# Kernel tuning notes

Hardware: AMD Instinct MI355X
Metric: run time of the kernel (lower is better)

Reference implementation:

```python
import jax, jax.numpy as jnp
import numpy as np


def rotary_pos_emb(x):
    # x: [b, h, l, k]; interleaved rotary embedding (pairs are (0,1),(2,3),...)
    dim = x.shape[-1]
    seq = x.shape[-2]
    ts = jnp.arange(0, dim, 2, dtype=jnp.float32)
    inv_freqs = 10000.0 ** (-ts / dim)                      # [dim/2]
    grid = jnp.arange(seq, dtype=jnp.float32)[:, None] * inv_freqs[None, :]  # [l, dim/2]
    sin_embs = jnp.repeat(jnp.sin(grid), 2, axis=-1)[None]  # [1, l, dim] (interleaved repeat)
    cos_embs = jnp.repeat(jnp.cos(grid), 2, axis=-1)[None]
    x1, x2 = x[..., ::2], x[..., 1::2]
    xs = jnp.stack([-x2, x1], axis=-1).reshape(x.shape)     # interleave (-x2, x1)
    return x * cos_embs + xs * sin_embs


def setup_inputs() -> dict:
    key = jax.random.key(0)
    ks = jax.random.split(key, 5)
    b, l, d = 2, 2048, 1024
    scale = 1.0 / np.sqrt(d)
    return {
        "x": jax.random.normal(ks[0], (b, l, d), dtype=jnp.float32),
        "Wq": jax.random.normal(ks[1], (d, d), dtype=jnp.float32) * scale,
        "Wk": jax.random.normal(ks[2], (d, d), dtype=jnp.float32) * scale,
        "Wv": jax.random.normal(ks[3], (d, d), dtype=jnp.float32) * scale,
        "Wo": jax.random.normal(ks[4], (d, d), dtype=jnp.float32) * scale,
        "is_training": 0,
    }


def reference(x, Wq, Wk, Wv, Wo, is_training):
    n_heads = 16
    b, l, d = x.shape
    k_size = d // n_heads
    # NOTE: module scales q by 1/sqrt(model_size), not 1/sqrt(key_size)
    q = (x @ Wq) / jnp.sqrt(jnp.float32(d))
    q = q.reshape(b, l, n_heads, k_size).transpose(0, 2, 1, 3)  # b h l k
    k = (x @ Wk).reshape(b, l, n_heads, k_size).transpose(0, 2, 1, 3)
    v = (x @ Wv).reshape(b, l, n_heads, k_size).transpose(0, 2, 1, 3)
    q = rotary_pos_emb(q)
    k = rotary_pos_emb(k)
    logits = jnp.einsum('bhik,bhjk->bhij', q, k)  # no mask, no dropout (eval)
    a = jax.nn.softmax(logits, axis=-1)
    y = jnp.einsum('bhij,bhjv->bhiv', a, v)
    y = y.transpose(0, 2, 1, 3).reshape(b, l, d)  # b l (h v)
    return y @ Wo
```

## Files before the change

kernel.cpp:

```cpp
#include <hip/hip_runtime.h>
#include <stdint.h>

typedef unsigned short u16;
typedef unsigned int u32;
using short8 = __attribute__((ext_vector_type(8))) short;
using f32x4  = __attribute__((ext_vector_type(4))) float;
using f32x16 = __attribute__((ext_vector_type(16))) float;

typedef __attribute__((address_space(1))) unsigned int gu32;
typedef __attribute__((address_space(3))) unsigned int lu32;

__device__ __forceinline__ void gl2lds16(const u16* g, u16* lds_wave_base) {
    __builtin_amdgcn_global_load_lds(
        (gu32*)(uintptr_t)(const void*)g,
        (lu32*)(uint32_t)(uintptr_t)(void*)lds_wave_base,
        16, 0, 0);
}

__device__ inline float bf2f(u16 u) {
    union { unsigned int i; float f; } v;
    v.i = ((unsigned int)u) << 16;
    return v.f;
}
__device__ inline u16 f2bf(float f) {
    union { float f; unsigned int i; } v;
    v.f = f;
    unsigned int x = v.i;
    return (u16)((x + 0x7fffu + ((x >> 16) & 1u)) >> 16);
}
__device__ inline u32 f2bf_trunc_u32(float f) {
    union { float f; unsigned int i; } v;
    v.f = f;
    return v.i >> 16;
}

__global__ __launch_bounds__(256) void prep(
    const float* __restrict__ x, u16* __restrict__ xb,
    const float* __restrict__ w0, const float* __restrict__ w1,
    const float* __restrict__ w2, const float* __restrict__ w3,
    u16* __restrict__ t0, u16* __restrict__ t1,
    u16* __restrict__ t2, u16* __restrict__ t3,
    float2* __restrict__ tab)
{
    int tx = threadIdx.x, ty = threadIdx.y;
    int tid = ty * 32 + tx;
    int z = blockIdx.z;
    if (z == 4) {
        int bidx = blockIdx.y * 32 + blockIdx.x;
        if (bidx < 256) {
            int idx = bidx * 256 + tid;
            int pos = idx >> 5, pi = idx & 31;
            const float l2_10000_over_32 = 0.41524101186f;
            float ang = (float)pos *
                __builtin_amdgcn_exp2f(-(float)pi * l2_10000_over_32);
            float sn, cs;
            __sincosf(ang, &sn, &cs);
            tab[idx] = make_float2(cs, sn);
        }
        return;
    }
    if (z >= 5) {
        int i = (((z - 5) * 1024 + blockIdx.y * 32 + blockIdx.x) * 256 + tid) * 4;
        float4 v = *(const float4*)(x + i);
        ushort4 o;
        o.x = f2bf(v.x); o.y = f2bf(v.y); o.z = f2bf(v.z); o.w = f2bf(v.w);
        *(ushort4*)(xb + i) = o;
        return;
    }
    __shared__ u16 tile[32][33];
    const float* src; u16* dst;
    switch (z) {
        case 0:  src = w0; dst = t0; break;
        case 1:  src = w1; dst = t1; break;
        case 2:  src = w2; dst = t2; break;
        default: src = w3; dst = t3; break;
    }
    int c0 = blockIdx.x * 32, r0 = blockIdx.y * 32;
    #pragma unroll
    for (int i = 0; i < 4; i++)
        tile[ty + i * 8][tx] = f2bf(src[(size_t)(r0 + ty + i * 8) * 1024 + c0 + tx]);
    __syncthreads();
    #pragma unroll
    for (int i = 0; i < 4; i++)
        dst[(size_t)(c0 + ty + i * 8) * 1024 + r0 + tx] = tile[tx][ty + i * 8];
}

__global__ __launch_bounds__(256) void gemm_qkv(
    const u16* __restrict__ A, const u16* __restrict__ Bt,
    const float2* __restrict__ ropetab,
    u16* __restrict__ Qb, u16* __restrict__ Kb, u16* __restrict__ VT)
{
    __shared__ __align__(16) char smem[24576];
    u16* As = (u16*)smem;
    u16* Bs = (u16*)(smem + 16384);

    const int tid  = threadIdx.x;
    const int lane = tid & 63;
    const int wid  = tid >> 6;
    const int quad = lane >> 4;
    const int l15  = lane & 15;
    const int wm   = wid >> 1, wn = wid & 1;

    const int m0 = blockIdx.y * 128;
    const int n0 = blockIdx.x * 64;
    const int mat = n0 >> 10;
    const int ln0 = n0 & 1023;

    f32x4 acc[4][2] = {};

    for (int k0 = 0; k0 < 1024; k0 += 64) {
        #pragma unroll
        for (int it = 0; it < 4; it++) {
            int c   = it * 256 + tid;
            int row = c >> 3;
            int col = ((c & 7) ^ (row & 7)) * 8;
            gl2lds16(&A[(size_t)(m0 + row) * 1024 + k0 + col],
                     &As[(size_t)(it * 256 + wid * 64) * 8]);
        }
        #pragma unroll
        for (int it = 0; it < 2; it++) {
            int c   = it * 256 + tid;
            int row = c >> 3;
            int col = ((c & 7) ^ (row & 7)) * 8;
            gl2lds16(&Bt[(size_t)(n0 + row) * 1024 + k0 + col],
                     &Bs[(size_t)(it * 256 + wid * 64) * 8]);
        }
        __syncthreads();

        #pragma unroll
        for (int s = 0; s < 2; s++) {
            short8 a[4], b[2];
            #pragma unroll
            for (int i = 0; i < 4; i++) {
                int ra = wm * 64 + i * 16 + l15;
                a[i] = *(const short8*)(&As[ra * 64 + (((s * 4 + quad) ^ (ra & 7)) * 8)]);
            }
            #pragma unroll
            for (int j = 0; j < 2; j++) {
                int rb = wn * 32 + j * 16 + l15;
                b[j] = *(const short8*)(&Bs[rb * 64 + (((s * 4 + quad) ^ (rb & 7)) * 8)]);
            }
            #pragma unroll
            for (int i = 0; i < 4; i++)
                #pragma unroll
                for (int j = 0; j < 2; j++)
                    acc[i][j] = __builtin_amdgcn_mfma_f32_16x16x32_bf16(a[i], b[j], acc[i][j], 0, 0, 0);
        }
        __syncthreads();
    }

    if (mat < 2) {
        u16* C = (mat == 0) ? Qb : Kb;
        const float scale = (mat == 0) ? (0.03125f * 1.44269504f) : 1.0f;
        const int odd = l15 & 1;
        #pragma unroll
        for (int i = 0; i < 4; i++)
            #pragma unroll
            for (int j = 0; j < 2; j++)
                #pragma unroll
                for (int r = 0; r < 4; r++) {
                    int lrow = wm * 64 + i * 16 + quad * 4 + r;
                    int col  = ln0 + wn * 32 + j * 16 + l15;
                    int pos  = (m0 + lrow) & 2047;
                    float v  = acc[i][j][r] * scale;
                    float vp = __shfl_xor(v, 1);
                    float2 sc = ropetab[pos * 32 + ((col & 63) >> 1)];
                    float outv = odd ? (v * sc.x + vp * sc.y)
                                     : (v * sc.x - vp * sc.y);
                    C[(size_t)(m0 + lrow) * 1024 + col] = f2bf(outv);
                }
    } else {
        u16* T = (u16*)smem;
        __syncthreads();
        const int qp = ((quad & 1) << 1) | (quad >> 1);
        #pragma unroll
        for (int i = 0; i < 4; i++)
            #pragma unroll
            for (int j = 0; j < 2; j++)
                #pragma unroll
                for (int r = 0; r < 4; r++) {
                    int prow = wm * 64 + i * 16 + qp * 4 + r;
                    int lcol = wn * 32 + j * 16 + l15;
                    T[lcol * 136 + prow] = f2bf(acc[i][j][r]);
                }
        __syncthreads();
        int bb2 = m0 >> 11, pos0 = m0 & 2047, h2 = ln0 >> 6;
        #pragma unroll
        for (int itc = 0; itc < 4; itc++) {
            int c  = itc * 256 + tid;
            int ch = c >> 4;
            int px = (c & 15) * 8;
            size_t dst = ((size_t)(bb2 * 16 + h2) * 64 + ch) * 2048
                         + pos0 + px;
            *(uint4*)(&VT[dst]) = *(const uint4*)(&T[ch * 136 + px]);
        }
    }
}

__global__ __launch_bounds__(256) void gemm_out(
    const u16* __restrict__ A, const u16* __restrict__ Bt, float* __restrict__ C)
{
    __shared__ __align__(16) u16 As[64 * 64];
    __shared__ __align__(16) u16 Bs[64 * 64];

    const int tid  = threadIdx.x;
    const int lane = tid & 63;
    const int wid  = tid >> 6;
    const int quad = lane >> 4;
    const int l15  = lane & 15;
    const int wm   = wid >> 1, wn = wid & 1;

    const int m0 = blockIdx.y * 64;
    const int n0 = blockIdx.x * 64;

    f32x4 acc[2][2] = {};

    for (int k0 = 0; k0 < 1024; k0 += 64) {
        #pragma unroll
        for (int it = 0; it < 2; it++) {
            int c   = it * 256 + tid;
            int row = c >> 3;
            int col = ((c & 7) ^ (row & 7)) * 8;
            gl2lds16(&A[(size_t)(m0 + row) * 1024 + k0 + col],
                     &As[(size_t)(it * 256 + wid * 64) * 8]);
        }
        #pragma unroll
        for (int it = 0; it < 2; it++) {
            int c   = it * 256 + tid;
            int row = c >> 3;
            int col = ((c & 7) ^ (row & 7)) * 8;
            gl2lds16(&Bt[(size_t)(n0 + row) * 1024 + k0 + col],
                     &Bs[(size_t)(it * 256 + wid * 64) * 8]);
        }
        __syncthreads();

        #pragma unroll
        for (int s = 0; s < 2; s++) {
            short8 a[2], b[2];
            #pragma unroll
            for (int i = 0; i < 2; i++) {
                int ra = wm * 32 + i * 16 + l15;
                a[i] = *(const short8*)(&As[ra * 64 + (((s * 4 + quad) ^ (ra & 7)) * 8)]);
            }
            #pragma unroll
            for (int j = 0; j < 2; j++) {
                int rb = wn * 32 + j * 16 + l15;
                b[j] = *(const short8*)(&Bs[rb * 64 + (((s * 4 + quad) ^ (rb & 7)) * 8)]);
            }
            #pragma unroll
            for (int i = 0; i < 2; i++)
                #pragma unroll
                for (int j = 0; j < 2; j++)
                    acc[i][j] = __builtin_amdgcn_mfma_f32_16x16x32_bf16(a[i], b[j], acc[i][j], 0, 0, 0);
        }
        __syncthreads();
    }

    #pragma unroll
    for (int i = 0; i < 2; i++)
        #pragma unroll
        for (int j = 0; j < 2; j++)
            #pragma unroll
            for (int r = 0; r < 4; r++) {
                int row = m0 + wm * 32 + i * 16 + quad * 4 + r;
                int col = n0 + wn * 32 + j * 16 + l15;
                C[(size_t)row * 1024 + col] = acc[i][j][r];
            }
}

__global__ __launch_bounds__(256, 2) void attn(
    const u16* __restrict__ Q, const u16* __restrict__ Kb,
    const u16* __restrict__ VT, u16* __restrict__ Y)
{
    __shared__ __align__(16) u16 Ks [128 * 68];
    __shared__ __align__(16) u16 VTs[64 * 128];

    const int tid  = threadIdx.x;
    const int lane = tid & 63, wid = tid >> 6;
    const int l31  = lane & 31, hi = lane >> 5;

    const int bh = blockIdx.x;
    const int qt = blockIdx.y;
    const int bb = bh >> 4, h = bh & 15;

    const size_t base = ((size_t)bb * 2048) * 1024 + (size_t)h * 64;

    short8 qf[4];
    {
        const u16* qp = Q + base
                      + ((size_t)qt * 128 + wid * 32 + l31) * 1024 + hi * 8;
        #pragma unroll
        for (int s = 0; s < 4; s++)
            qf[s] = *(const short8*)(qp + s * 16);
    }

    const int c0 = tid,        c1 = 256 + tid,
              c2 = 512 + tid,  c3 = 768 + tid;
    const int rk0 = c0 >> 3, ck0 = ((c0 & 7) ^ (rk0 & 7)) * 8;
    const int rk1 = c1 >> 3, ck1 = ((c1 & 7) ^ (rk1 & 7)) * 8;
    const int rk2 = c2 >> 3, ck2 = ((c2 & 7) ^ (rk2 & 7)) * 8;
    const int rk3 = c3 >> 3, ck3 = ((c3 & 7) ^ (rk3 & 7)) * 8;
    const int rv0 = c0 >> 4, cv0 = ((c0 & 15) ^ (rv0 & 15)) * 8;
    const int rv1 = c1 >> 4, cv1 = ((c1 & 15) ^ (rv1 & 15)) * 8;
    const int rv2 = c2 >> 4, cv2 = ((c2 & 15) ^ (rv2 & 15)) * 8;
    const int rv3 = c3 >> 4, cv3 = ((c3 & 15) ^ (rv3 & 15)) * 8;
    const int dK0 = rk0 * 68 + (c0 & 7) * 8, dK1 = rk1 * 68 + (c1 & 7) * 8;
    const int dK2 = rk2 * 68 + (c2 & 7) * 8, dK3 = rk3 * 68 + (c3 & 7) * 8;
    const u16* pK = Kb + base;
    const u16* pV = VT + ((size_t)bh * 64) * 2048;
    const size_t oK0 = (size_t)rk0 * 1024 + ck0, oK1 = (size_t)rk1 * 1024 + ck1;
    const size_t oK2 = (size_t)rk2 * 1024 + ck2, oK3 = (size_t)rk3 * 1024 + ck3;
    const size_t oV0 = (size_t)rv0 * 2048 + cv0, oV1 = (size_t)rv1 * 2048 + cv1;
    const size_t oV2 = (size_t)rv2 * 2048 + cv2, oV3 = (size_t)rv3 * 2048 + cv3;

    uint4 k0r, k1r, k2r, k3r, v0r, v1r, v2r, v3r;
#define LOADREGS(J0)                                                        \
    do {                                                                    \
        const size_t jk = (size_t)(J0) * 1024;                              \
        k0r = *(const uint4*)(pK + jk + oK0);                               \
        k1r = *(const uint4*)(pK + jk + oK1);                               \
        k2r = *(const uint4*)(pK + jk + oK2);                               \
        k3r = *(const uint4*)(pK + jk + oK3);                               \
        v0r = *(const uint4*)(pV + (J0) + oV0);                             \
        v1r = *(const uint4*)(pV + (J0) + oV1);                             \
        v2r = *(const uint4*)(pV + (J0) + oV2);                             \
        v3r = *(const uint4*)(pV + (J0) + oV3);                             \
    } while (0)

    f32x16 o0 = {}, o1 = {};
    float lsum = 0.0f;

    LOADREGS(0);

    for (int j0 = 0; j0 < 2048; j0 += 128) {
        __syncthreads();
        *(uint4*)(&Ks [dK0]) = k0r;
        *(uint4*)(&Ks [dK1]) = k1r;
        *(uint4*)(&Ks [dK2]) = k2r;
        *(uint4*)(&Ks [dK3]) = k3r;
        *(uint4*)(&VTs[(0 * 256 + tid) * 8]) = v0r;
        *(uint4*)(&VTs[(1 * 256 + tid) * 8]) = v1r;
        *(uint4*)(&VTs[(2 * 256 + tid) * 8]) = v2r;
        *(uint4*)(&VTs[(3 * 256 + tid) * 8]) = v3r;
        if (j0 + 128 < 2048)
            LOADREGS(j0 + 128);
        __syncthreads();

        f32x16 st[4];
        #pragma unroll
        for (int t = 0; t < 4; t++) {
            int key = t * 32 + l31;
            f32x16 z = {};
            __builtin_amdgcn_s_setprio(1);
            #pragma unroll
            for (int s = 0; s < 4; s++) {
                int chunk = ((2 * s + hi) ^ (key & 7)) * 8;
                short8 kf = *(const short8*)(&Ks[key * 68 + chunk]);
                z = __builtin_amdgcn_mfma_f32_32x32x16_bf16(kf, qf[s], z, 0, 0, 0);
            }
            __builtin_amdgcn_s_setprio(0);
            st[t] = z;
        }

        u32 X[4][4], Y[4][4];
        #pragma unroll
        for (int t = 0; t < 4; t++)
            #pragma unroll
            for (int g = 0; g < 4; g++) {
                float p0 = __builtin_amdgcn_exp2f(st[t][4 * g + 0]);
                float p1 = __builtin_amdgcn_exp2f(st[t][4 * g + 1]);
                float p2 = __builtin_amdgcn_exp2f(st[t][4 * g + 2]);
                float p3 = __builtin_amdgcn_exp2f(st[t][4 * g + 3]);
                lsum += (p0 + p1) + (p2 + p3);
                X[t][g] = f2bf_trunc_u32(p0) | (f2bf_trunc_u32(p1) << 16);
                Y[t][g] = f2bf_trunc_u32(p2) | (f2bf_trunc_u32(p3) << 16);
            }

        #pragma unroll
        for (int c16 = 0; c16 < 8; ++c16) {
            const int t = c16 >> 1, u = c16 & 1;
            union { u32 u4[4]; short8 s8; } pk;
            pk.u4[0] = X[t][2 * u];
            pk.u4[1] = Y[t][2 * u];
            pk.u4[2] = X[t][2 * u + 1];
            pk.u4[3] = Y[t][2 * u + 1];
            const int kch = 2 * c16 + hi;
            short8 v0 = *(const short8*)(&VTs[l31 * 128 + ((kch ^ (l31 & 15)) * 8)]);
            short8 v1 = *(const short8*)(&VTs[(32 + l31) * 128 + ((kch ^ ((32 + l31) & 15)) * 8)]);
            __builtin_amdgcn_s_setprio(1);
            o0 = __builtin_amdgcn_mfma_f32_32x32x16_bf16(pk.s8, v0, o0, 0, 0, 0);
            o1 = __builtin_amdgcn_mfma_f32_32x32x16_bf16(pk.s8, v1, o1, 0, 0, 0);
            __builtin_amdgcn_s_setprio(0);
        }
    }
#undef LOADREGS

    lsum += __shfl_xor(lsum, 32);
    float linv = 1.0f / lsum;

    size_t qrow0 = (size_t)qt * 128 + wid * 32;
    #pragma unroll
    for (int half = 0; half < 2; half++) {
        f32x16 o = half ? o1 : o0;
        #pragma unroll
        for (int reg = 0; reg < 16; reg++) {
            int qrow = (reg & 3) + 8 * (reg >> 2) + 4 * hi;
            float nv = o[reg] * __shfl(linv, qrow);
            Y[base + (qrow0 + qrow) * 1024 + half * 32 + l31] = f2bf(nv);
        }
    }
}

extern "C" void kernel_launch(void* const* d_in, const int* in_sizes, int n_in,
                              void* d_out, int out_size, void* d_ws, size_t ws_size,
                              hipStream_t stream)
{
    const float* x  = (const float*)d_in[0];
    const float* Wq = (const float*)d_in[1];
    const float* Wk = (const float*)d_in[2];
    const float* Wv = (const float*)d_in[3];
    const float* Wo = (const float*)d_in[4];
    float* out = (float*)d_out;

    char* ws = (char*)d_ws;
    u16*    xb    = (u16*)   (ws + (0ull  << 20));
    u16*    WqkvT = (u16*)   (ws + (8ull  << 20));
    u16*    WoT   = (u16*)   (ws + (14ull << 20));
    u16*    Qb    = (u16*)   (ws + (16ull << 20));
    u16*    Kb    = (u16*)   (ws + (24ull << 20));
    u16*    VTb   = (u16*)   (ws + (32ull << 20));
    u16*    Yb    = (u16*)   (ws + (40ull << 20));
    float2* tab   = (float2*)(ws + (48ull << 20));

    prep<<<dim3(32, 32, 9), dim3(32, 8), 0, stream>>>(
        x, xb, Wq, Wk, Wv, Wo,
        WqkvT, WqkvT + (1024ull * 1024), WqkvT + (2048ull * 1024), WoT, tab);
    gemm_qkv<<<dim3(48, 32), 256, 0, stream>>>(xb, WqkvT, tab, Qb, Kb, VTb);
    attn<<<dim3(32, 16), 256, 0, stream>>>(Qb, Kb, VTb, Yb);
    gemm_out<<<dim3(16, 64), 256, 0, stream>>>(Yb, WoT, out);
}
```

Baseline: 181.7 us.

## Double-buffer K/V tiles in LDS to halve barriers in attention loop

```diff
diff --git a/kernel.cpp b/kernel.cpp
--- a/kernel.cpp
+++ b/kernel.cpp
@@ -272,8 +272,10 @@
     const u16* __restrict__ Q, const u16* __restrict__ Kb,
     const u16* __restrict__ VT, u16* __restrict__ Y)
 {
-    __shared__ __align__(16) u16 Ks [128 * 68];
-    __shared__ __align__(16) u16 VTs[64 * 128];
+    __shared__ __align__(16) u16 Ks0 [128 * 68];
+    __shared__ __align__(16) u16 Ks1 [128 * 68];
+    __shared__ __align__(16) u16 VTs0[64 * 128];
+    __shared__ __align__(16) u16 VTs1[64 * 128];
 
     const int tid  = threadIdx.x;
     const int lane = tid & 63, wid = tid >> 6;
@@ -330,22 +332,18 @@
     f32x16 o0 = {}, o1 = {};
     float lsum = 0.0f;
 
-    LOADREGS(0);
-
-    for (int j0 = 0; j0 < 2048; j0 += 128) {
-        __syncthreads();
-        *(uint4*)(&Ks [dK0]) = k0r;
-        *(uint4*)(&Ks [dK1]) = k1r;
-        *(uint4*)(&Ks [dK2]) = k2r;
-        *(uint4*)(&Ks [dK3]) = k3r;
-        *(uint4*)(&VTs[(0 * 256 + tid) * 8]) = v0r;
-        *(uint4*)(&VTs[(1 * 256 + tid) * 8]) = v1r;
-        *(uint4*)(&VTs[(2 * 256 + tid) * 8]) = v2r;
-        *(uint4*)(&VTs[(3 * 256 + tid) * 8]) = v3r;
-        if (j0 + 128 < 2048)
-            LOADREGS(j0 + 128);
-        __syncthreads();
-
+    auto stage_w = [&](u16* KS, u16* VS) {
+        *(uint4*)(&KS[dK0]) = k0r;
+        *(uint4*)(&KS[dK1]) = k1r;
+        *(uint4*)(&KS[dK2]) = k2r;
+        *(uint4*)(&KS[dK3]) = k3r;
+        *(uint4*)(&VS[(0 * 256 + tid) * 8]) = v0r;
+        *(uint4*)(&VS[(1 * 256 + tid) * 8]) = v1r;
+        *(uint4*)(&VS[(2 * 256 + tid) * 8]) = v2r;
+        *(uint4*)(&VS[(3 * 256 + tid) * 8]) = v3r;
+    };
+
+    auto compute_tile = [&](const u16* KS, const u16* VS) {
         f32x16 st[4];
         #pragma unroll
         for (int t = 0; t < 4; t++) {
@@ -355,14 +353,14 @@
             #pragma unroll
             for (int s = 0; s < 4; s++) {
                 int chunk = ((2 * s + hi) ^ (key & 7)) * 8;
-                short8 kf = *(const short8*)(&Ks[key * 68 + chunk]);
+                short8 kf = *(const short8*)(&KS[key * 68 + chunk]);
                 z = __builtin_amdgcn_mfma_f32_32x32x16_bf16(kf, qf[s], z, 0, 0, 0);
             }
             __builtin_amdgcn_s_setprio(0);
             st[t] = z;
         }
 
-        u32 X[4][4], Y[4][4];
+        u32 X[4][4], Y2[4][4];
         #pragma unroll
         for (int t = 0; t < 4; t++)
             #pragma unroll
@@ -372,26 +370,45 @@
                 float p2 = __builtin_amdgcn_exp2f(st[t][4 * g + 2]);
                 float p3 = __builtin_amdgcn_exp2f(st[t][4 * g + 3]);
                 lsum += (p0 + p1) + (p2 + p3);
-                X[t][g] = f2bf_trunc_u32(p0) | (f2bf_trunc_u32(p1) << 16);
-                Y[t][g] = f2bf_trunc_u32(p2) | (f2bf_trunc_u32(p3) << 16);
+                X [t][g] = f2bf_trunc_u32(p0) | (f2bf_trunc_u32(p1) << 16);
+                Y2[t][g] = f2bf_trunc_u32(p2) | (f2bf_trunc_u32(p3) << 16);
             }
 
         #pragma unroll
         for (int c16 = 0; c16 < 8; ++c16) {
             const int t = c16 >> 1, u = c16 & 1;
             union { u32 u4[4]; short8 s8; } pk;
-            pk.u4[0] = X[t][2 * u];
-            pk.u4[1] = Y[t][2 * u];
-            pk.u4[2] = X[t][2 * u + 1];
-            pk.u4[3] = Y[t][2 * u + 1];
+            pk.u4[0] = X [t][2 * u];
+            pk.u4[1] = Y2[t][2 * u];
+            pk.u4[2] = X [t][2 * u + 1];
+            pk.u4[3] = Y2[t][2 * u + 1];
             const int kch = 2 * c16 + hi;
-            short8 v0 = *(const short8*)(&VTs[l31 * 128 + ((kch ^ (l31 & 15)) * 8)]);
-            short8 v1 = *(const short8*)(&VTs[(32 + l31) * 128 + ((kch ^ ((32 + l31) & 15)) * 8)]);
+            short8 v0 = *(const short8*)(&VS[l31 * 128 + ((kch ^ (l31 & 15)) * 8)]);
+            short8 v1 = *(const short8*)(&VS[(32 + l31) * 128 + ((kch ^ ((32 + l31) & 15)) * 8)]);
             __builtin_amdgcn_s_setprio(1);
             o0 = __builtin_amdgcn_mfma_f32_32x32x16_bf16(pk.s8, v0, o0, 0, 0, 0);
             o1 = __builtin_amdgcn_mfma_f32_32x32x16_bf16(pk.s8, v1, o1, 0, 0, 0);
             __builtin_amdgcn_s_setprio(0);
         }
+    };
+
+    LOADREGS(0);
+    stage_w(Ks0, VTs0);
+    LOADREGS(128);
+    __syncthreads();
+
+    for (int j0 = 0; j0 < 2048; j0 += 256) {
+        stage_w(Ks1, VTs1);
+        if (j0 + 256 < 2048) LOADREGS(j0 + 256);
+        compute_tile(Ks0, VTs0);
+        __syncthreads();
+
+        if (j0 + 256 < 2048) {
+            stage_w(Ks0, VTs0);
+            if (j0 + 384 < 2048) LOADREGS(j0 + 384);
+        }
+        compute_tile(Ks1, VTs1);
+        __syncthreads();
     }
 #undef LOADREGS
 
```

Result: slower. 221.1 us (+21.7%).
